# Kernel tuning notes

Measured on AMD Instinct MI355X. Metric: run time of the kernel, lower is better.

The kernel has to match this reference:

```python
import jax, jax.numpy as jnp
import numpy as np

E = 128       # embed_size
H = 256       # hidden_size
Q = 256       # query_size
B = 256       # batch size
N_ENT = 200000
N_REL = 500
N_NODES = 100000   # existing (head) nodes
N_NEW = 50000      # new tail nodes (segment_sum size)
M = 200000         # edges


def setup_inputs() -> dict:
    key = jax.random.key(0)
    ks = jax.random.split(key, 32)
    s = 0.02
    inp = {
        'entity_emb':   jax.random.normal(ks[0], (N_ENT, E), jnp.float32),
        'relation_emb': jax.random.normal(ks[1], (N_REL, E), jnp.float32),
        'node_hidden':  jax.random.normal(ks[2], (N_NODES, H), jnp.float32),
        'query_repr':   jax.random.normal(ks[3], (B, Q), jnp.float32),
        # attention params (Ws_attn, Wr_attn, Wqr_attn, w_alpha)
        'Ws':  jax.random.normal(ks[4], (H, H), jnp.float32) * s,
        'Wr':  jax.random.normal(ks[5], (E, H), jnp.float32) * s,
        'Wqr': jax.random.normal(ks[6], (E, H), jnp.float32) * s,
        'bqr': jnp.zeros((H,), jnp.float32),
        'w_alpha': jax.random.normal(ks[7], (H, 1), jnp.float32) * s,
        'b_alpha': jnp.zeros((1,), jnp.float32),
        # GRUCell (input = 2E message, hidden = H), torch layout [3H, in]
        'W_ih': jax.random.normal(ks[8], (3 * H, 2 * E), jnp.float32) * s,
        'W_hh': jax.random.normal(ks[9], (3 * H, H), jnp.float32) * s,
        'b_ih': jnp.zeros((3 * H,), jnp.float32),
        'b_hh': jnp.zeros((3 * H,), jnp.float32),
        # We2h: entity embed -> initial hidden
        'We2h_W': jax.random.normal(ks[10], (E, H), jnp.float32) * s,
        'We2h_b': jnp.zeros((H,), jnp.float32),
        # candidate_layer: [2E + H] -> H (agent_num = 1)
        'cand_W': jax.random.normal(ks[11], (2 * E + H, H), jnp.float32) * s,
        'cand_b': jnp.zeros((H,), jnp.float32),
        # rank_layer: [H + Q] -> 1
        'rank_W': jax.random.normal(ks[12], (H + Q, 1), jnp.float32) * s,
        'rank_b': jnp.zeros((1,), jnp.float32),
        # LayerNorm
        'ln_g': jnp.ones((H,), jnp.float32),
        'ln_b': jnp.zeros((H,), jnp.float32),
        # edge list (int constants)
        'head_node':     jax.random.randint(ks[13], (M,), 0, N_NODES, jnp.int32),
        'edge_rel':      jax.random.randint(ks[14], (M,), 0, N_REL, jnp.int32),
        'tail_ent':      jax.random.randint(ks[15], (M,), 0, N_ENT, jnp.int32),
        'tail_node':     jax.random.randint(ks[16], (M,), 0, N_NEW, jnp.int32),
        'query_rel':     jax.random.randint(ks[17], (M,), 0, N_REL, jnp.int32),
        'batch_idx':     jax.random.randint(ks[18], (M,), 0, B, jnp.int32),
        'tail_node_ent': jax.random.randint(ks[19], (N_NEW,), 0, N_ENT, jnp.int32),
    }
    return inp


def reference(entity_emb, relation_emb, node_hidden, query_repr,
              Ws, Wr, Wqr, bqr, w_alpha, b_alpha,
              W_ih, W_hh, b_ih, b_hh, We2h_W, We2h_b,
              cand_W, cand_b, rank_W, rank_b, ln_g, ln_b,
              head_node, edge_rel, tail_ent, tail_node, query_rel,
              batch_idx, tail_node_ent):
    lrelu = lambda x: jax.nn.leaky_relu(x, 0.01)
    # --- per-edge attention: w_alpha(ReLU(Ws h_s + Wr h_r + Wqr h_q)) ---
    hs = node_hidden[head_node]            # [M, H]
    hr = relation_emb[edge_rel]            # [M, E]
    hq = relation_emb[query_rel]           # [M, E]
    attn_feat = jax.nn.relu(hs @ Ws + hr @ Wr + hq @ Wqr + bqr)   # [M, H]
    alpha = jax.nn.sigmoid(attn_feat @ w_alpha + b_alpha)         # [M, 1]
    # --- attention-weighted message (rel || tail entity) scattered to tails ---
    te = entity_emb[tail_ent]                                     # [M, E]
    msg = jnp.concatenate([hr, te], axis=-1) * alpha              # [M, 2E]
    agg = jax.ops.segment_sum(msg, tail_node, num_segments=N_NEW) # [N_NEW, 2E]
    # --- GRUCell update of tail-node hidden states ---
    h_prev = lrelu(entity_emb[tail_node_ent] @ We2h_W + We2h_b)   # [N_NEW, H]
    gx = agg @ W_ih.T + b_ih                                      # [N_NEW, 3H]
    gh = h_prev @ W_hh.T + b_hh
    xr, xz, xn = jnp.split(gx, 3, axis=-1)
    hr_, hz_, hn_ = jnp.split(gh, 3, axis=-1)
    r = jax.nn.sigmoid(xr + hr_)
    z = jax.nn.sigmoid(xz + hz_)
    n = jnp.tanh(xn + r * hn_)
    h_new = (1.0 - z) * n + z * h_prev                            # [N_NEW, H]
    mu = jnp.mean(h_new, axis=-1, keepdims=True)
    var = jnp.var(h_new, axis=-1, keepdims=True)
    h_new = (h_new - mu) * jax.lax.rsqrt(var + 1e-5) * ln_g + ln_b
    # --- candidate scoring: candidate_layer + rank_layer ---
    cand_in = jnp.concatenate([te, hr, h_new[tail_node]], axis=-1)   # [M, 2E+H]
    cand_h = lrelu(cand_in @ cand_W + cand_b)                        # [M, H]
    rank_in = jnp.concatenate([cand_h, query_repr[batch_idx]], -1)   # [M, H+Q]
    scores = (rank_in @ rank_W + rank_b)[:, 0]                       # [M]
    return scores
```

## Files before the change

### kernel.cpp

```cpp
#include <hip/hip_runtime.h>
#include <math.h>


#define ACT_NONE 0
#define ACT_LRELU 1

typedef __attribute__((ext_vector_type(8))) short short8;
typedef __attribute__((ext_vector_type(4))) float floatx4;

__device__ __forceinline__ ushort f2b(float x) {
    union { float f; unsigned u; } v; v.f = x;
    return (ushort)((v.u + 0x7fffu + ((v.u >> 16) & 1u)) >> 16);
}
__device__ __forceinline__ float b2f(ushort b) {
    union { unsigned u; float f; } v; v.u = ((unsigned)b) << 16;
    return v.f;
}
__device__ __forceinline__ void gload16(const ushort* g, ushort* l) {
    __builtin_amdgcn_global_load_lds(
        (const __attribute__((address_space(1))) void*)g,
        (__attribute__((address_space(3))) void*)l, 16, 0, 0);
}

__global__ __launch_bounds__(256) void gemm_k(
    const float* __restrict__ A, const float* __restrict__ B,
    const float* __restrict__ bias, float* __restrict__ C,
    int M, int N, int K, const int* __restrict__ a_idx, int act)
{
    __shared__ float As[16][68];
    __shared__ float Bs[16][68];
    const int tid = threadIdx.x;
    const int tx = tid & 15, ty = tid >> 4;
    const int m0 = blockIdx.x * 64, n0 = blockIdx.y * 64;
    float acc[4][4] = {};
    const int ar  = tid >> 2;
    const int ac4 = (tid & 3) * 4;
    const int brow = tid >> 4;
    const int bc4  = (tid & 15) * 4;
    const int gm = m0 + ar;
    const float* Arow = nullptr;
    if (gm < M) {
        int r = a_idx ? a_idx[gm] : gm;
        Arow = A + (size_t)r * K;
    }
    for (int k0 = 0; k0 < K; k0 += 16) {
        float4 av = make_float4(0.f, 0.f, 0.f, 0.f);
        if (Arow) av = *(const float4*)(Arow + k0 + ac4);
        As[ac4 + 0][ar] = av.x;
        As[ac4 + 1][ar] = av.y;
        As[ac4 + 2][ar] = av.z;
        As[ac4 + 3][ar] = av.w;
        float4 bv = *(const float4*)(B + (size_t)(k0 + brow) * N + n0 + bc4);
        *(float4*)&Bs[brow][bc4] = bv;
        __syncthreads();
        #pragma unroll
        for (int kk = 0; kk < 16; ++kk) {
            float4 a4 = *(float4*)&As[kk][ty << 2];
            float4 b4 = *(float4*)&Bs[kk][tx << 2];
            float avr[4] = {a4.x, a4.y, a4.z, a4.w};
            float bvr[4] = {b4.x, b4.y, b4.z, b4.w};
            #pragma unroll
            for (int i = 0; i < 4; ++i)
                #pragma unroll
                for (int j = 0; j < 4; ++j)
                    acc[i][j] = fmaf(avr[i], bvr[j], acc[i][j]);
        }
        __syncthreads();
    }
    const int n = n0 + (tx << 2);
    float4 bv4 = make_float4(0.f, 0.f, 0.f, 0.f);
    if (bias) bv4 = *(const float4*)(bias + n);
    #pragma unroll
    for (int i = 0; i < 4; ++i) {
        int m = m0 + (ty << 2) + i;
        if (m >= M) continue;
        float v0 = acc[i][0] + bv4.x;
        float v1 = acc[i][1] + bv4.y;
        float v2 = acc[i][2] + bv4.z;
        float v3 = acc[i][3] + bv4.w;
        if (act == ACT_LRELU) {
            v0 = v0 > 0.f ? v0 : 0.01f * v0;
            v1 = v1 > 0.f ? v1 : 0.01f * v1;
            v2 = v2 > 0.f ? v2 : 0.01f * v2;
            v3 = v3 > 0.f ? v3 : 0.01f * v3;
        }
        *(float4*)(C + (size_t)m * N + n) = make_float4(v0, v1, v2, v3);
    }
}

__global__ __launch_bounds__(256) void convert16_k(
    const float* __restrict__ in, ushort* __restrict__ out, int n)
{
    int i = blockIdx.x * 256 + threadIdx.x;
    if (i < n) out[i] = f2b(in[i]);
}

__global__ __launch_bounds__(256) void transpose16_k(
    const float* __restrict__ in, ushort* __restrict__ out, int k0, int KS, int N)
{
    int i = blockIdx.x * 256 + threadIdx.x;
    if (i >= KS * N) return;
    int k = i / N, n = i - k * N;
    out[(size_t)n * KS + k] = f2b(in[(size_t)(k0 + k) * N + n]);
}

__global__ __launch_bounds__(256) void gemm16_k(
    const float* __restrict__ A, const int* __restrict__ a_idx,
    const ushort* __restrict__ A16,
    const ushort* __restrict__ BT, const float* __restrict__ bias,
    float* __restrict__ C, ushort* __restrict__ C16,
    int M, int N, int K, int act)
{
    __shared__ ushort As[128 * 40];
    __shared__ ushort Bs[128 * 40];
    const int tid = threadIdx.x;
    const int m0 = blockIdx.x * 128, n0 = blockIdx.y * 128;

    const int rowbase = tid >> 3, f4 = tid & 7;
    const float* arow[4] = {nullptr, nullptr, nullptr, nullptr};
    const int rb16 = tid >> 2, seg16 = tid & 3;
    const ushort* a16row[2] = {nullptr, nullptr};
    if (A16) {
        #pragma unroll
        for (int i = 0; i < 2; ++i) {
            int r = m0 + rb16 + i * 64;
            if (r < M) {
                int rr = a_idx ? a_idx[r] : r;
                a16row[i] = A16 + (size_t)rr * K;
            }
        }
    } else {
        #pragma unroll
        for (int i = 0; i < 4; ++i) {
            int r = m0 + rowbase + i * 32;
            if (r < M) {
                int rr = a_idx ? a_idx[r] : r;
                arow[i] = A + (size_t)rr * K;
            }
        }
    }
    const int brow = tid >> 2, bseg = tid & 3;

    const int l = tid & 63, w = tid >> 6;
    const int wm = (w & 1) * 64, wn = (w >> 1) * 64;
    const int cl = l & 15, q = l >> 4;
    const int aoff = (wm + cl) * 40 + q * 8;
    const int boff = (wn + cl) * 40 + q * 8;

    floatx4 acc[4][4];
    #pragma unroll
    for (int mi = 0; mi < 4; ++mi)
        #pragma unroll
        for (int ni = 0; ni < 4; ++ni) acc[mi][ni] = 0.f;

    for (int k0 = 0; k0 < K; k0 += 32) {
        if (A16) {
            #pragma unroll
            for (int i = 0; i < 2; ++i) {
                uint4 raw = make_uint4(0u, 0u, 0u, 0u);
                if (a16row[i]) raw = *(const uint4*)(a16row[i] + k0 + seg16 * 8);
                *(uint4*)&As[(rb16 + i * 64) * 40 + seg16 * 8] = raw;
            }
        } else {
            #pragma unroll
            for (int i = 0; i < 4; ++i) {
                float4 v = make_float4(0.f, 0.f, 0.f, 0.f);
                if (arow[i]) v = *(const float4*)(arow[i] + k0 + f4 * 4);
                ushort4 b4;
                b4.x = f2b(v.x); b4.y = f2b(v.y); b4.z = f2b(v.z); b4.w = f2b(v.w);
                *(ushort4*)&As[(rowbase + i * 32) * 40 + f4 * 4] = b4;
            }
        }
        #pragma unroll
        for (int i = 0; i < 2; ++i) {
            int r = brow + i * 64;
            uint4 raw = *(const uint4*)(BT + (size_t)(n0 + r) * K + k0 + bseg * 8);
            *(uint4*)&Bs[r * 40 + bseg * 8] = raw;
        }
        __syncthreads();
        short8 af[4], bf[4];
        #pragma unroll
        for (int mi = 0; mi < 4; ++mi) af[mi] = *(short8*)&As[aoff + mi * 640];
        #pragma unroll
        for (int ni = 0; ni < 4; ++ni) bf[ni] = *(short8*)&Bs[boff + ni * 640];
        #pragma unroll
        for (int mi = 0; mi < 4; ++mi)
            #pragma unroll
            for (int ni = 0; ni < 4; ++ni)
                acc[mi][ni] = __builtin_amdgcn_mfma_f32_16x16x32_bf16(
                    bf[ni], af[mi], acc[mi][ni], 0, 0, 0);
        __syncthreads();
    }

    #pragma unroll
    for (int mi = 0; mi < 4; ++mi) {
        int row = m0 + wm + mi * 16 + cl;
        if (row >= M) continue;
        #pragma unroll
        for (int ni = 0; ni < 4; ++ni) {
            int col = n0 + wn + ni * 16 + q * 4;
            float4 bv = bias ? *(const float4*)(bias + col)
                             : make_float4(0.f, 0.f, 0.f, 0.f);
            float v[4];
            #pragma unroll
            for (int r = 0; r < 4; ++r) {
                float x = acc[mi][ni][r] + ((const float*)&bv)[r];
                if (act == ACT_LRELU) x = x > 0.f ? x : 0.01f * x;
                v[r] = x;
            }
            if (C16) {
                ushort4 u;
                u.x = f2b(v[0]); u.y = f2b(v[1]); u.z = f2b(v[2]); u.w = f2b(v[3]);
                *(ushort4*)(C16 + (size_t)row * N + col) = u;
            }
            if (C) *(float4*)(C + (size_t)row * N + col) =
                       make_float4(v[0], v[1], v[2], v[3]);
        }
    }
}

__global__ __launch_bounds__(256) void gemm16p_k(
    const ushort* __restrict__ A16, const int* __restrict__ a_idx,
    const ushort* __restrict__ BT, const float* __restrict__ bias,
    float* __restrict__ C, ushort* __restrict__ C16,
    int M, int N, int K, int act)
{
    __shared__ ushort As[2][128 * 32];
    __shared__ ushort Bs[2][128 * 32];
    const int tid = threadIdx.x;
    const int l = tid & 63, w = tid >> 6;
    const int m0 = blockIdx.y * 128, n0 = blockIdx.x * 128;

    const ushort* agp[2];
    const ushort* bgp[2];
    #pragma unroll
    for (int j = 0; j < 2; ++j) {
        int row = j * 64 + w * 16 + (l >> 2);
        int seg = (l & 3) ^ (row & 3);
        int r = m0 + row; if (r >= M) r = M - 1;
        int rr = a_idx ? a_idx[r] : r;
        agp[j] = A16 + (size_t)rr * K + seg * 8;
        bgp[j] = BT + (size_t)(n0 + row) * K + seg * 8;
    }

    const int wm = (w & 1) * 64, wn = (w >> 1) * 64;
    const int cl = l & 15, q = l >> 4;
    const int sseg = (q ^ (cl & 3)) * 8;
    const int aoff = (wm + cl) * 32 + sseg;
    const int boff = (wn + cl) * 32 + sseg;

    floatx4 acc[4][4];
    #pragma unroll
    for (int mi = 0; mi < 4; ++mi)
        #pragma unroll
        for (int ni = 0; ni < 4; ++ni) acc[mi][ni] = 0.f;

    const int NT = K >> 5;
    #pragma unroll
    for (int j = 0; j < 2; ++j) {
        gload16(agp[j], &As[0][j * 2048 + w * 512]);
        gload16(bgp[j], &Bs[0][j * 2048 + w * 512]);
    }
    __syncthreads();

    int buf = 0;
    for (int t = 0; t < NT; ++t) {
        if (t + 1 < NT) {
            int k0 = (t + 1) * 32;
            #pragma unroll
            for (int j = 0; j < 2; ++j) {
                gload16(agp[j] + k0, &As[buf ^ 1][j * 2048 + w * 512]);
                gload16(bgp[j] + k0, &Bs[buf ^ 1][j * 2048 + w * 512]);
            }
        }
        short8 af[4], bf[4];
        #pragma unroll
        for (int mi = 0; mi < 4; ++mi) af[mi] = *(short8*)&As[buf][aoff + mi * 512];
        #pragma unroll
        for (int ni = 0; ni < 4; ++ni) bf[ni] = *(short8*)&Bs[buf][boff + ni * 512];
        #pragma unroll
        for (int mi = 0; mi < 4; ++mi)
            #pragma unroll
            for (int ni = 0; ni < 4; ++ni)
                acc[mi][ni] = __builtin_amdgcn_mfma_f32_16x16x32_bf16(
                    bf[ni], af[mi], acc[mi][ni], 0, 0, 0);
        __syncthreads();
        buf ^= 1;
    }

    #pragma unroll
    for (int mi = 0; mi < 4; ++mi) {
        int row = m0 + wm + mi * 16 + cl;
        if (row >= M) continue;
        #pragma unroll
        for (int ni = 0; ni < 4; ++ni) {
            int col = n0 + wn + ni * 16 + q * 4;
            float4 bv = bias ? *(const float4*)(bias + col)
                             : make_float4(0.f, 0.f, 0.f, 0.f);
            float v[4];
            #pragma unroll
            for (int r = 0; r < 4; ++r) {
                float x = acc[mi][ni][r] + ((const float*)&bv)[r];
                if (act == ACT_LRELU) x = x > 0.f ? x : 0.01f * x;
                v[r] = x;
            }
            if (C16) {
                ushort4 u;
                u.x = f2b(v[0]); u.y = f2b(v[1]); u.z = f2b(v[2]); u.w = f2b(v[3]);
                *(ushort4*)(C16 + (size_t)row * N + col) = u;
            }
            if (C) *(float4*)(C + (size_t)row * N + col) =
                       make_float4(v[0], v[1], v[2], v[3]);
        }
    }
}

__global__ __launch_bounds__(256) void qdot_k(
    const float* __restrict__ q, const float* __restrict__ rank_W,
    float* __restrict__ qdot)
{
    int b = blockIdx.x * 4 + (threadIdx.x >> 6);
    int l = threadIdx.x & 63;
    float s = 0.f;
    #pragma unroll
    for (int k = 0; k < 4; ++k) {
        int h = l + k * 64;
        s += q[(size_t)b * 256 + h] * rank_W[256 + h];
    }
    #pragma unroll
    for (int off = 32; off; off >>= 1) s += __shfl_xor(s, off, 64);
    if (l == 0) qdot[b] = s;
}

__global__ __launch_bounds__(256) void alpha_k(
    const ushort* __restrict__ nodeWs16, const float* __restrict__ relWr,
    const float* __restrict__ relWqr, const float* __restrict__ bqr,
    const float* __restrict__ w_alpha, const float* __restrict__ b_alpha_p,
    const int* __restrict__ head_node, const int* __restrict__ edge_rel,
    const int* __restrict__ query_rel, float* __restrict__ alpha_out)
{
    const int tid = threadIdx.x;
    const int e0 = blockIdx.x * 32;
    __shared__ int hn[32], er[32], qr[32];
    if (tid < 32) {
        int e = e0 + tid;
        hn[tid] = head_node[e]; er[tid] = edge_rel[e]; qr[tid] = query_rel[e];
    }
    __syncthreads();
    const int tx = tid & 63, ty = tid >> 6;
    const int c = tx * 4;
    const float4 bq = *(const float4*)(bqr + c);
    const float4 wa = *(const float4*)(w_alpha + c);
    float part[8];
    #pragma unroll
    for (int i2 = 0; i2 < 8; ++i2) {
        int i = ty * 8 + i2;
        ushort4 a16 = *(const ushort4*)(nodeWs16 + (size_t)hn[i] * 256 + c);
        float4 b = *(const float4*)(relWr + (size_t)er[i] * 256 + c);
        float4 d = *(const float4*)(relWqr + (size_t)qr[i] * 256 + c);
        float x0 = fmaxf(b2f(a16.x) + b.x + d.x + bq.x, 0.f);
        float x1 = fmaxf(b2f(a16.y) + b.y + d.y + bq.y, 0.f);
        float x2 = fmaxf(b2f(a16.z) + b.z + d.z + bq.z, 0.f);
        float x3 = fmaxf(b2f(a16.w) + b.w + d.w + bq.w, 0.f);
        part[i2] = x0 * wa.x + x1 * wa.y + x2 * wa.z + x3 * wa.w;
    }
    #pragma unroll
    for (int off = 32; off; off >>= 1)
        #pragma unroll
        for (int i2 = 0; i2 < 8; ++i2)
            part[i2] += __shfl_xor(part[i2], off, 64);
    if (tx == 0) {
        float ba = b_alpha_p[0];
        #pragma unroll
        for (int i2 = 0; i2 < 8; ++i2)
            alpha_out[e0 + ty * 8 + i2] = 1.f / (1.f + __expf(-(part[i2] + ba)));
    }
}

__global__ __launch_bounds__(256) void hist_k(
    const int* __restrict__ tail_node, int* __restrict__ deg, int M)
{
    int e = blockIdx.x * 256 + threadIdx.x;
    if (e < M) atomicAdd(&deg[tail_node[e]], 1);
}
__global__ __launch_bounds__(256) void scan1_k(
    const int* __restrict__ deg, int* __restrict__ partial, int N)
{
    __shared__ int sm[256];
    int i = blockIdx.x * 256 + threadIdx.x;
    int v = (i < N) ? deg[i] : 0;
    sm[threadIdx.x] = v;
    __syncthreads();
    for (int off = 128; off; off >>= 1) {
        if (threadIdx.x < off) sm[threadIdx.x] += sm[threadIdx.x + off];
        __syncthreads();
    }
    if (threadIdx.x == 0) partial[blockIdx.x] = sm[0];
}
__global__ __launch_bounds__(256) void scan2_k(
    int* __restrict__ partial, int nPart, int* __restrict__ offsets, int N, int M)
{
    __shared__ int sm[256];
    int t = threadIdx.x;
    int v = (t < nPart) ? partial[t] : 0;
    sm[t] = v;
    __syncthreads();
    for (int off = 1; off < 256; off <<= 1) {
        int add = (t >= off) ? sm[t - off] : 0;
        __syncthreads();
        sm[t] += add;
        __syncthreads();
    }
    if (t < nPart) partial[t] = sm[t] - v;
    if (t == 0) offsets[N] = M;
}
__global__ __launch_bounds__(256) void scan3_k(
    const int* __restrict__ deg, const int* __restrict__ partial,
    int* __restrict__ offsets, int* __restrict__ cursor, int N)
{
    __shared__ int sm[256];
    int i = blockIdx.x * 256 + threadIdx.x;
    int t = threadIdx.x;
    int v = (i < N) ? deg[i] : 0;
    sm[t] = v;
    __syncthreads();
    for (int off = 1; off < 256; off <<= 1) {
        int add = (t >= off) ? sm[t - off] : 0;
        __syncthreads();
        sm[t] += add;
        __syncthreads();
    }
    if (i < N) {
        int excl = partial[blockIdx.x] + sm[t] - v;
        offsets[i] = excl;
        cursor[i] = excl;
    }
}
__global__ __launch_bounds__(256) void fill_k(
    const int* __restrict__ tail_node, int* __restrict__ cursor,
    int* __restrict__ csr, int M)
{
    int e = blockIdx.x * 256 + threadIdx.x;
    if (e < M) {
        int pos = atomicAdd(&cursor[tail_node[e]], 1);
        csr[pos] = e;
    }
}

__global__ __launch_bounds__(256) void agg_csr_k(
    const float* __restrict__ relation_emb, const ushort* __restrict__ ent16,
    const float* __restrict__ alpha, const int* __restrict__ edge_rel,
    const int* __restrict__ tail_ent, const int* __restrict__ offsets,
    const int* __restrict__ csr, ushort* __restrict__ agg16)
{
    int node = blockIdx.x * 4 + (threadIdx.x >> 6);
    int lane = threadIdx.x & 63;
    int beg = offsets[node], end = offsets[node + 1];
    float4 acc = make_float4(0.f, 0.f, 0.f, 0.f);
    const int c = lane * 4;
    for (int j = beg; j < end; ++j) {
        int e = csr[j];
        float a = alpha[e];
        float4 v;
        if (lane < 32) {
            v = *(const float4*)(relation_emb + (size_t)edge_rel[e] * 128 + c);
        } else {
            ushort4 u = *(const ushort4*)(ent16 + (size_t)tail_ent[e] * 128 + (c - 128));
            v = make_float4(b2f(u.x), b2f(u.y), b2f(u.z), b2f(u.w));
        }
        acc.x += v.x * a; acc.y += v.y * a;
        acc.z += v.z * a; acc.w += v.w * a;
    }
    ushort4 o;
    o.x = f2b(acc.x); o.y = f2b(acc.y); o.z = f2b(acc.z); o.w = f2b(acc.w);
    *(ushort4*)(agg16 + (size_t)node * 256 + c) = o;
}

__global__ __launch_bounds__(256) void gru_ln_k(
    const float* __restrict__ gx, const float* __restrict__ gh,
    const float* __restrict__ h_prev, const float* __restrict__ ln_g,
    const float* __restrict__ ln_b, ushort* __restrict__ h_new16, int n0)
{
    int nl = blockIdx.x * 4 + (threadIdx.x >> 6);
    int lane = threadIdx.x & 63;
    int n = n0 + nl;
    const float* gxr = gx + (size_t)nl * 768;
    const float* ghr = gh + (size_t)nl * 768;
    const float* hpr = h_prev + (size_t)n * 256;
    float hv[4]; float s = 0.f, s2 = 0.f;
    #pragma unroll
    for (int q2 = 0; q2 < 4; ++q2) {
        int h = lane + q2 * 64;
        float xr = gxr[h], xz = gxr[256 + h], xn = gxr[512 + h];
        float hr_ = ghr[h], hz_ = ghr[256 + h], hn_ = ghr[512 + h];
        float hp = hpr[h];
        float r = 1.f / (1.f + __expf(-(xr + hr_)));
        float z = 1.f / (1.f + __expf(-(xz + hz_)));
        float nn = tanhf(xn + r * hn_);
        float v = (1.f - z) * nn + z * hp;
        hv[q2] = v; s += v; s2 += v * v;
    }
    #pragma unroll
    for (int off = 32; off; off >>= 1) {
        s  += __shfl_xor(s, off, 64);
        s2 += __shfl_xor(s2, off, 64);
    }
    float mean = s * (1.f / 256.f);
    float var  = s2 * (1.f / 256.f) - mean * mean;
    float rstd = rsqrtf(var + 1e-5f);
    ushort* outr = h_new16 + (size_t)n * 256;
    #pragma unroll
    for (int q2 = 0; q2 < 4; ++q2) {
        int h = lane + q2 * 64;
        outr[h] = f2b((hv[q2] - mean) * rstd * ln_g[h] + ln_b[h]);
    }
}

__global__ __launch_bounds__(256) void score_mfma_k(
    const ushort* __restrict__ ent16, const ushort* __restrict__ candW1T,
    const ushort* __restrict__ relCand16, const ushort* __restrict__ hnewCand16,
    const float* __restrict__ rank_W, const float* __restrict__ rank_b_p,
    const float* __restrict__ qdot, const int* __restrict__ csr,
    const int* __restrict__ tail_ent, const int* __restrict__ edge_rel,
    const int* __restrict__ tail_node, const int* __restrict__ batch_idx,
    float* __restrict__ scores)
{
    __shared__ ushort As[64 * 136];
    __shared__ int s_e[64], s_te[64], s_er[64], s_tn[64], s_bi[64];
    __shared__ float s_part[4][64];
    const int tid = threadIdx.x;
    const int e0 = blockIdx.x * 64;
    if (tid < 64) {
        int e = csr[e0 + tid];
        s_e[tid] = e;
        s_te[tid] = tail_ent[e]; s_er[tid] = edge_rel[e];
        s_tn[tid] = tail_node[e]; s_bi[tid] = batch_idx[e];
    }
    __syncthreads();

    {
        const int row = tid >> 2, s0 = tid & 3;
        const ushort* ar = ent16 + (size_t)s_te[row] * 128;
        #pragma unroll
        for (int j = 0; j < 4; ++j) {
            int seg = s0 + j * 4;
            *(uint4*)&As[row * 136 + seg * 8] = *(const uint4*)(ar + seg * 8);
        }
    }
    __syncthreads();

    const int l = tid & 63, w = tid >> 6;
    const int cl = l & 15, q = l >> 4;

    floatx4 acc[4][4];
    #pragma unroll
    for (int mi = 0; mi < 4; ++mi)
        #pragma unroll
        for (int ni = 0; ni < 4; ++ni) acc[mi][ni] = 0.f;

    const ushort* bbase = candW1T + (size_t)(w * 64 + cl) * 128 + q * 8;

    for (int k0 = 0; k0 < 128; k0 += 32) {
        short8 af[4], bf[4];
        #pragma unroll
        for (int ni = 0; ni < 4; ++ni)
            bf[ni] = *(const short8*)(bbase + ni * 2048 + k0);
        #pragma unroll
        for (int mi = 0; mi < 4; ++mi)
            af[mi] = *(short8*)&As[(mi * 16 + cl) * 136 + k0 + q * 8];
        #pragma unroll
        for (int mi = 0; mi < 4; ++mi)
            #pragma unroll
            for (int ni = 0; ni < 4; ++ni)
                acc[mi][ni] = __builtin_amdgcn_mfma_f32_16x16x32_bf16(
                    bf[ni], af[mi], acc[mi][ni], 0, 0, 0);
    }

    float rowsum[4];
    #pragma unroll
    for (int mi = 0; mi < 4; ++mi) {
        int row = mi * 16 + cl;
        int er = s_er[row], tn = s_tn[row];
        float rs = 0.f;
        #pragma unroll
        for (int ni = 0; ni < 4; ++ni) {
            int col = w * 64 + ni * 16 + q * 4;
            ushort4 rc = *(const ushort4*)(relCand16 + (size_t)er * 256 + col);
            ushort4 hc = *(const ushort4*)(hnewCand16 + (size_t)tn * 256 + col);
            float4 rw = *(const float4*)(rank_W + col);
            float v0 = acc[mi][ni][0] + b2f(rc.x) + b2f(hc.x);
            float v1 = acc[mi][ni][1] + b2f(rc.y) + b2f(hc.y);
            float v2 = acc[mi][ni][2] + b2f(rc.z) + b2f(hc.z);
            float v3 = acc[mi][ni][3] + b2f(rc.w) + b2f(hc.w);
            v0 = v0 > 0.f ? v0 : 0.01f * v0;
            v1 = v1 > 0.f ? v1 : 0.01f * v1;
            v2 = v2 > 0.f ? v2 : 0.01f * v2;
            v3 = v3 > 0.f ? v3 : 0.01f * v3;
            rs += v0 * rw.x + v1 * rw.y + v2 * rw.z + v3 * rw.w;
        }
        rowsum[mi] = rs;
    }
    #pragma unroll
    for (int mi = 0; mi < 4; ++mi) {
        rowsum[mi] += __shfl_xor(rowsum[mi], 16, 64);
        rowsum[mi] += __shfl_xor(rowsum[mi], 32, 64);
    }
    if (q == 0) {
        #pragma unroll
        for (int mi = 0; mi < 4; ++mi)
            s_part[w][mi * 16 + cl] = rowsum[mi];
    }
    __syncthreads();
    if (tid < 64) {
        float s = s_part[0][tid] + s_part[1][tid] + s_part[2][tid] + s_part[3][tid]
                + qdot[s_bi[tid]] + rank_b_p[0];
        scores[s_e[tid]] = s;
    }
}

extern "C" void kernel_launch(void* const* d_in, const int* in_sizes, int n_in,
                              void* d_out, int out_size, void* d_ws, size_t ws_size,
                              hipStream_t stream)
{
    const float* entity_emb   = (const float*)d_in[0];
    const float* relation_emb = (const float*)d_in[1];
    const float* node_hidden  = (const float*)d_in[2];
    const float* query_repr   = (const float*)d_in[3];
    const float* Ws    = (const float*)d_in[4];
    const float* Wr    = (const float*)d_in[5];
    const float* Wqr   = (const float*)d_in[6];
    const float* bqr   = (const float*)d_in[7];
    const float* w_alpha = (const float*)d_in[8];
    const float* b_alpha = (const float*)d_in[9];
    const float* W_ih  = (const float*)d_in[10];
    const float* W_hh  = (const float*)d_in[11];
    const float* b_ih  = (const float*)d_in[12];
    const float* b_hh  = (const float*)d_in[13];
    const float* We2h_W = (const float*)d_in[14];
    const float* We2h_b = (const float*)d_in[15];
    const float* cand_W = (const float*)d_in[16];
    const float* cand_b = (const float*)d_in[17];
    const float* rank_W = (const float*)d_in[18];
    const float* rank_b = (const float*)d_in[19];
    const float* ln_g  = (const float*)d_in[20];
    const float* ln_b  = (const float*)d_in[21];
    const int* head_node = (const int*)d_in[22];
    const int* edge_rel  = (const int*)d_in[23];
    const int* tail_ent  = (const int*)d_in[24];
    const int* tail_node = (const int*)d_in[25];
    const int* query_rel = (const int*)d_in[26];
    const int* batch_idx = (const int*)d_in[27];
    const int* tail_node_ent = (const int*)d_in[28];
    float* out = (float*)d_out;
    (void)in_sizes; (void)n_in; (void)out_size; (void)ws_size;

    const int M = 200000, NNEW = 50000, NNODES = 100000, NREL = 500;
    const int NENT = 200000, E = 128;
    const int NCHUNK = 4, NC = NNEW / NCHUNK;
    const int NPART = (NNEW + 255) / 256;

    float* w = (float*)d_ws;
    float* relWr    = w; w += NREL * 256;
    float* relWqr   = w; w += NREL * 256;
    float* relCand  = w; w += NREL * 256;
    float* qdot     = w; w += 256;
    float* alpha    = w; w += M;
    float* h_prev   = w; w += (size_t)NNEW * 256;
    ushort* agg16      = (ushort*)w; w += (size_t)NNEW * 256 / 2;
    ushort* hnewCand16 = (ushort*)w; w += (size_t)NNEW * 256 / 2;
    ushort* relCand16  = (ushort*)w; w += (NREL * 256) / 2;
    ushort* ent16      = (ushort*)w; w += (size_t)NENT * E / 2;
    ushort* h_new16    = (ushort*)w; w += (size_t)NNEW * 256 / 2;
    ushort* W_ih16    = (ushort*)w; w += (768 * 256) / 2;
    ushort* W_hh16    = (ushort*)w; w += (768 * 256) / 2;
    ushort* WsT16     = (ushort*)w; w += (256 * 256) / 2;
    ushort* We2hT16   = (ushort*)w; w += (256 * 128) / 2;
    ushort* candW1T16 = (ushort*)w; w += (256 * 128) / 2;
    ushort* candW3T16 = (ushort*)w; w += (256 * 256) / 2;
    int* deg     = (int*)w; w += NNEW;
    int* offsets = (int*)w; w += NNEW + 1;
    int* cursor  = (int*)w; w += NNEW;
    int* partial = (int*)w; w += 256;
    int* csr     = (int*)w; w += M;
    w = (float*)(((uintptr_t)w + 63) & ~(uintptr_t)63);
    float* big = w;
    ushort* nh16     = (ushort*)big;
    ushort* nodeWs16 = (ushort*)big + (size_t)NNODES * 256;
    float* gx_buf = big;
    float* gh_buf = big + (size_t)NC * 768;

    hipMemsetAsync(deg, 0, NNEW * sizeof(int), stream);
    hist_k<<<(M + 255) / 256, 256, 0, stream>>>(tail_node, deg, M);
    scan1_k<<<NPART, 256, 0, stream>>>(deg, partial, NNEW);
    scan2_k<<<1, 256, 0, stream>>>(partial, NPART, offsets, NNEW, M);
    scan3_k<<<NPART, 256, 0, stream>>>(deg, partial, offsets, cursor, NNEW);
    fill_k<<<(M + 255) / 256, 256, 0, stream>>>(tail_node, cursor, csr, M);

    convert16_k<<<(NENT * E + 255) / 256, 256, 0, stream>>>(entity_emb, ent16, NENT * E);
    convert16_k<<<(NNODES * 256 + 255) / 256, 256, 0, stream>>>(node_hidden, nh16, NNODES * 256);
    convert16_k<<<768, 256, 0, stream>>>(W_ih, W_ih16, 768 * 256);
    convert16_k<<<768, 256, 0, stream>>>(W_hh, W_hh16, 768 * 256);
    transpose16_k<<<256, 256, 0, stream>>>(Ws, WsT16, 0, 256, 256);
    transpose16_k<<<128, 256, 0, stream>>>(We2h_W, We2hT16, 0, 128, 256);
    transpose16_k<<<128, 256, 0, stream>>>(cand_W, candW1T16, 0, 128, 256);
    transpose16_k<<<256, 256, 0, stream>>>(cand_W, candW3T16, 256, 256, 256);
    gemm_k<<<dim3(8, 4), 256, 0, stream>>>(relation_emb, Wr,  nullptr, relWr,  NREL, 256, 128, nullptr, ACT_NONE);
    gemm_k<<<dim3(8, 4), 256, 0, stream>>>(relation_emb, Wqr, nullptr, relWqr, NREL, 256, 128, nullptr, ACT_NONE);
    gemm_k<<<dim3(8, 4), 256, 0, stream>>>(relation_emb, cand_W + 128 * 256, nullptr, relCand, NREL, 256, 128, nullptr, ACT_NONE);
    convert16_k<<<(NREL * 256 + 255) / 256, 256, 0, stream>>>(relCand, relCand16, NREL * 256);
    qdot_k<<<64, 256, 0, stream>>>(query_repr, rank_W, qdot);

    gemm16p_k<<<dim3(2, (NNODES + 127) / 128), 256, 0, stream>>>(
        nh16, nullptr, WsT16, nullptr, nullptr, nodeWs16, NNODES, 256, 256, ACT_NONE);

    alpha_k<<<M / 32, 256, 0, stream>>>(nodeWs16, relWr, relWqr, bqr, w_alpha, b_alpha,
                                        head_node, edge_rel, query_rel, alpha);

    agg_csr_k<<<NNEW / 4, 256, 0, stream>>>(relation_emb, ent16, alpha,
                                            edge_rel, tail_ent, offsets, csr, agg16);

    gemm16p_k<<<dim3(2, (NNEW + 127) / 128), 256, 0, stream>>>(
        ent16, tail_node_ent, We2hT16, We2h_b, h_prev, nullptr, NNEW, 256, 128, ACT_LRELU);

    for (int ch = 0; ch < NCHUNK; ++ch) {
        int n0 = ch * NC;
        gemm16p_k<<<dim3(6, (NC + 127) / 128), 256, 0, stream>>>(
            agg16 + (size_t)n0 * 256, nullptr, W_ih16, b_ih, gx_buf, nullptr, NC, 768, 256, ACT_NONE);
        gemm16_k<<<dim3((NC + 127) / 128, 6), 256, 0, stream>>>(
            h_prev + (size_t)n0 * 256, nullptr, nullptr, W_hh16, b_hh, gh_buf, nullptr, NC, 768, 256, ACT_NONE);
        gru_ln_k<<<NC / 4, 256, 0, stream>>>(gx_buf, gh_buf, h_prev, ln_g, ln_b, h_new16, n0);
    }

    gemm16p_k<<<dim3(2, (NNEW + 127) / 128), 256, 0, stream>>>(
        h_new16, nullptr, candW3T16, cand_b, nullptr, hnewCand16, NNEW, 256, 256, ACT_NONE);

    score_mfma_k<<<M / 64, 256, 0, stream>>>(ent16, candW1T16, relCand16, hnewCand16,
                                             rank_W, rank_b, qdot, csr, tail_ent,
                                             edge_rel, tail_node, batch_idx, out);
}
```

Baseline: 915.8 us.

## Sort edges by head node, store GRU intermediates in bf16, fuse fp32 convert into GEMM

Builds a second CSR keyed on head node so alpha_k gathers nodeWs rows in sorted order, and materializes permuted edge attributes so later kernels read them sequentially. Replaces the separate node_hidden bf16 conversion with a GEMM that converts fp32 A tiles on the fly. Stores h_prev, gx and gh in bf16 and runs the W_hh GEMM through the pipelined kernel. It also widens the scan blocks and reworks score_mfma_k to handle 128 edges per block. The aim is less memory traffic and better gather locality, at the cost of extra sort passes and lower intermediate precision.

```diff
diff --git a/kernel.cpp b/kernel.cpp
--- a/kernel.cpp
+++ b/kernel.cpp
@@ -94,7 +94,6 @@
     int i = blockIdx.x * 256 + threadIdx.x;
     if (i < n) out[i] = f2b(in[i]);
 }
-
 __global__ __launch_bounds__(256) void transpose16_k(
     const float* __restrict__ in, ushort* __restrict__ out, int k0, int KS, int N)
 {
@@ -104,48 +103,35 @@
     out[(size_t)n * KS + k] = f2b(in[(size_t)(k0 + k) * N + n]);
 }
 
-__global__ __launch_bounds__(256) void gemm16_k(
-    const float* __restrict__ A, const int* __restrict__ a_idx,
-    const ushort* __restrict__ A16,
+__global__ __launch_bounds__(256) void gemm16p_k(
+    const ushort* __restrict__ A16, const int* __restrict__ a_idx,
     const ushort* __restrict__ BT, const float* __restrict__ bias,
     float* __restrict__ C, ushort* __restrict__ C16,
     int M, int N, int K, int act)
 {
-    __shared__ ushort As[128 * 40];
-    __shared__ ushort Bs[128 * 40];
+    __shared__ ushort As[2][128 * 32];
+    __shared__ ushort Bs[2][128 * 32];
     const int tid = threadIdx.x;
-    const int m0 = blockIdx.x * 128, n0 = blockIdx.y * 128;
-
-    const int rowbase = tid >> 3, f4 = tid & 7;
-    const float* arow[4] = {nullptr, nullptr, nullptr, nullptr};
-    const int rb16 = tid >> 2, seg16 = tid & 3;
-    const ushort* a16row[2] = {nullptr, nullptr};
-    if (A16) {
-        #pragma unroll
-        for (int i = 0; i < 2; ++i) {
-            int r = m0 + rb16 + i * 64;
-            if (r < M) {
-                int rr = a_idx ? a_idx[r] : r;
-                a16row[i] = A16 + (size_t)rr * K;
-            }
-        }
-    } else {
-        #pragma unroll
-        for (int i = 0; i < 4; ++i) {
-            int r = m0 + rowbase + i * 32;
-            if (r < M) {
-                int rr = a_idx ? a_idx[r] : r;
-                arow[i] = A + (size_t)rr * K;
-            }
-        }
-    }
-    const int brow = tid >> 2, bseg = tid & 3;
-
     const int l = tid & 63, w = tid >> 6;
+    const int m0 = blockIdx.y * 128, n0 = blockIdx.x * 128;
+
+    const ushort* agp[2];
+    const ushort* bgp[2];
+    #pragma unroll
+    for (int j = 0; j < 2; ++j) {
+        int row = j * 64 + w * 16 + (l >> 2);
+        int seg = (l & 3) ^ (row & 3);
+        int r = m0 + row; if (r >= M) r = M - 1;
+        int rr = a_idx ? a_idx[r] : r;
+        agp[j] = A16 + (size_t)rr * K + seg * 8;
+        bgp[j] = BT + (size_t)(n0 + row) * K + seg * 8;
+    }
+
     const int wm = (w & 1) * 64, wn = (w >> 1) * 64;
     const int cl = l & 15, q = l >> 4;
-    const int aoff = (wm + cl) * 40 + q * 8;
-    const int boff = (wn + cl) * 40 + q * 8;
+    const int sseg = (q ^ (cl & 3)) * 8;
+    const int aoff = (wm + cl) * 32 + sseg;
+    const int boff = (wn + cl) * 32 + sseg;
 
     floatx4 acc[4][4];
     #pragma unroll
@@ -153,36 +139,29 @@
         #pragma unroll
         for (int ni = 0; ni < 4; ++ni) acc[mi][ni] = 0.f;
 
-    for (int k0 = 0; k0 < K; k0 += 32) {
-        if (A16) {
-            #pragma unroll
-            for (int i = 0; i < 2; ++i) {
-                uint4 raw = make_uint4(0u, 0u, 0u, 0u);
-                if (a16row[i]) raw = *(const uint4*)(a16row[i] + k0 + seg16 * 8);
-                *(uint4*)&As[(rb16 + i * 64) * 40 + seg16 * 8] = raw;
+    const int NT = K >> 5;
+    #pragma unroll
+    for (int j = 0; j < 2; ++j) {
+        gload16(agp[j], &As[0][j * 2048 + w * 512]);
+        gload16(bgp[j], &Bs[0][j * 2048 + w * 512]);
+    }
+    __syncthreads();
+
+    int buf = 0;
+    for (int t = 0; t < NT; ++t) {
+        if (t + 1 < NT) {
+            int k0 = (t + 1) * 32;
+            #pragma unroll
+            for (int j = 0; j < 2; ++j) {
+                gload16(agp[j] + k0, &As[buf ^ 1][j * 2048 + w * 512]);
+                gload16(bgp[j] + k0, &Bs[buf ^ 1][j * 2048 + w * 512]);
             }
-        } else {
-            #pragma unroll
-            for (int i = 0; i < 4; ++i) {
-                float4 v = make_float4(0.f, 0.f, 0.f, 0.f);
-                if (arow[i]) v = *(const float4*)(arow[i] + k0 + f4 * 4);
-                ushort4 b4;
-                b4.x = f2b(v.x); b4.y = f2b(v.y); b4.z = f2b(v.z); b4.w = f2b(v.w);
-                *(ushort4*)&As[(rowbase + i * 32) * 40 + f4 * 4] = b4;
-            }
-        }
-        #pragma unroll
-        for (int i = 0; i < 2; ++i) {
-            int r = brow + i * 64;
-            uint4 raw = *(const uint4*)(BT + (size_t)(n0 + r) * K + k0 + bseg * 8);
-            *(uint4*)&Bs[r * 40 + bseg * 8] = raw;
-        }
-        __syncthreads();
+        }
         short8 af[4], bf[4];
         #pragma unroll
-        for (int mi = 0; mi < 4; ++mi) af[mi] = *(short8*)&As[aoff + mi * 640];
-        #pragma unroll
-        for (int ni = 0; ni < 4; ++ni) bf[ni] = *(short8*)&Bs[boff + ni * 640];
+        for (int mi = 0; mi < 4; ++mi) af[mi] = *(short8*)&As[buf][aoff + mi * 512];
+        #pragma unroll
+        for (int ni = 0; ni < 4; ++ni) bf[ni] = *(short8*)&Bs[buf][boff + ni * 512];
         #pragma unroll
         for (int mi = 0; mi < 4; ++mi)
             #pragma unroll
@@ -190,6 +169,7 @@
                 acc[mi][ni] = __builtin_amdgcn_mfma_f32_16x16x32_bf16(
                     bf[ni], af[mi], acc[mi][ni], 0, 0, 0);
         __syncthreads();
+        buf ^= 1;
     }
 
     #pragma unroll
@@ -219,10 +199,9 @@
     }
 }
 
-__global__ __launch_bounds__(256) void gemm16p_k(
-    const ushort* __restrict__ A16, const int* __restrict__ a_idx,
-    const ushort* __restrict__ BT, const float* __restrict__ bias,
-    float* __restrict__ C, ushort* __restrict__ C16,
+__global__ __launch_bounds__(256) void gemm16pf_k(
+    const float* __restrict__ A, const ushort* __restrict__ BT,
+    const float* __restrict__ bias, ushort* __restrict__ C16,
     int M, int N, int K, int act)
 {
     __shared__ ushort As[2][128 * 32];
@@ -231,15 +210,21 @@
     const int l = tid & 63, w = tid >> 6;
     const int m0 = blockIdx.y * 128, n0 = blockIdx.x * 128;
 
-    const ushort* agp[2];
+    const int rowbase = tid >> 3, f4 = tid & 7;
+    const float* arow[4];
+    int awadr[4];
+    #pragma unroll
+    for (int i = 0; i < 4; ++i) {
+        int row = rowbase + i * 32;
+        int r = m0 + row; if (r >= M) r = M - 1;
+        arow[i] = A + (size_t)r * K;
+        awadr[i] = row * 32 + (((f4 >> 1) ^ (row & 3)) * 8) + (f4 & 1) * 4;
+    }
     const ushort* bgp[2];
     #pragma unroll
     for (int j = 0; j < 2; ++j) {
         int row = j * 64 + w * 16 + (l >> 2);
         int seg = (l & 3) ^ (row & 3);
-        int r = m0 + row; if (r >= M) r = M - 1;
-        int rr = a_idx ? a_idx[r] : r;
-        agp[j] = A16 + (size_t)rr * K + seg * 8;
         bgp[j] = BT + (size_t)(n0 + row) * K + seg * 8;
     }
 
@@ -257,21 +242,26 @@
 
     const int NT = K >> 5;
     #pragma unroll
-    for (int j = 0; j < 2; ++j) {
-        gload16(agp[j], &As[0][j * 2048 + w * 512]);
-        gload16(bgp[j], &Bs[0][j * 2048 + w * 512]);
+    for (int j = 0; j < 2; ++j) gload16(bgp[j], &Bs[0][j * 2048 + w * 512]);
+    #pragma unroll
+    for (int i = 0; i < 4; ++i) {
+        float4 v = *(const float4*)(arow[i] + f4 * 4);
+        ushort4 u; u.x = f2b(v.x); u.y = f2b(v.y); u.z = f2b(v.z); u.w = f2b(v.w);
+        *(ushort4*)&As[0][awadr[i]] = u;
     }
     __syncthreads();
 
     int buf = 0;
     for (int t = 0; t < NT; ++t) {
+        float4 av[4];
         if (t + 1 < NT) {
             int k0 = (t + 1) * 32;
             #pragma unroll
-            for (int j = 0; j < 2; ++j) {
-                gload16(agp[j] + k0, &As[buf ^ 1][j * 2048 + w * 512]);
+            for (int j = 0; j < 2; ++j)
                 gload16(bgp[j] + k0, &Bs[buf ^ 1][j * 2048 + w * 512]);
-            }
+            #pragma unroll
+            for (int i = 0; i < 4; ++i)
+                av[i] = *(const float4*)(arow[i] + k0 + f4 * 4);
         }
         short8 af[4], bf[4];
         #pragma unroll
@@ -284,6 +274,15 @@
             for (int ni = 0; ni < 4; ++ni)
                 acc[mi][ni] = __builtin_amdgcn_mfma_f32_16x16x32_bf16(
                     bf[ni], af[mi], acc[mi][ni], 0, 0, 0);
+        if (t + 1 < NT) {
+            #pragma unroll
+            for (int i = 0; i < 4; ++i) {
+                ushort4 u;
+                u.x = f2b(av[i].x); u.y = f2b(av[i].y);
+                u.z = f2b(av[i].z); u.w = f2b(av[i].w);
+                *(ushort4*)&As[buf ^ 1][awadr[i]] = u;
+            }
+        }
         __syncthreads();
         buf ^= 1;
     }
@@ -297,20 +296,19 @@
             int col = n0 + wn + ni * 16 + q * 4;
             float4 bv = bias ? *(const float4*)(bias + col)
                              : make_float4(0.f, 0.f, 0.f, 0.f);
-            float v[4];
-            #pragma unroll
-            for (int r = 0; r < 4; ++r) {
-                float x = acc[mi][ni][r] + ((const float*)&bv)[r];
-                if (act == ACT_LRELU) x = x > 0.f ? x : 0.01f * x;
-                v[r] = x;
+            ushort4 u;
+            float x0 = acc[mi][ni][0] + bv.x;
+            float x1 = acc[mi][ni][1] + bv.y;
+            float x2 = acc[mi][ni][2] + bv.z;
+            float x3 = acc[mi][ni][3] + bv.w;
+            if (act == ACT_LRELU) {
+                x0 = x0 > 0.f ? x0 : 0.01f * x0;
+                x1 = x1 > 0.f ? x1 : 0.01f * x1;
+                x2 = x2 > 0.f ? x2 : 0.01f * x2;
+                x3 = x3 > 0.f ? x3 : 0.01f * x3;
             }
-            if (C16) {
-                ushort4 u;
-                u.x = f2b(v[0]); u.y = f2b(v[1]); u.z = f2b(v[2]); u.w = f2b(v[3]);
-                *(ushort4*)(C16 + (size_t)row * N + col) = u;
-            }
-            if (C) *(float4*)(C + (size_t)row * N + col) =
-                       make_float4(v[0], v[1], v[2], v[3]);
+            u.x = f2b(x0); u.y = f2b(x1); u.z = f2b(x2); u.w = f2b(x3);
+            *(ushort4*)(C16 + (size_t)row * N + col) = u;
         }
     }
 }
@@ -336,15 +334,17 @@
     const ushort* __restrict__ nodeWs16, const float* __restrict__ relWr,
     const float* __restrict__ relWqr, const float* __restrict__ bqr,
     const float* __restrict__ w_alpha, const float* __restrict__ b_alpha_p,
-    const int* __restrict__ head_node, const int* __restrict__ edge_rel,
-    const int* __restrict__ query_rel, float* __restrict__ alpha_out)
+    const int* __restrict__ hcsr_hn, const int* __restrict__ hcsr_er,
+    const int* __restrict__ hcsr_qr, const int* __restrict__ hcsr_e,
+    float* __restrict__ alpha_out)
 {
     const int tid = threadIdx.x;
     const int e0 = blockIdx.x * 32;
-    __shared__ int hn[32], er[32], qr[32];
+    __shared__ int hn[32], er[32], qr[32], se[32];
     if (tid < 32) {
-        int e = e0 + tid;
-        hn[tid] = head_node[e]; er[tid] = edge_rel[e]; qr[tid] = query_rel[e];
+        int i = e0 + tid;
+        hn[tid] = hcsr_hn[i]; er[tid] = hcsr_er[i];
+        qr[tid] = hcsr_qr[i]; se[tid] = hcsr_e[i];
     }
     __syncthreads();
     const int tx = tid & 63, ty = tid >> 6;
@@ -373,25 +373,24 @@
         float ba = b_alpha_p[0];
         #pragma unroll
         for (int i2 = 0; i2 < 8; ++i2)
-            alpha_out[e0 + ty * 8 + i2] = 1.f / (1.f + __expf(-(part[i2] + ba)));
+            alpha_out[se[ty * 8 + i2]] = 1.f / (1.f + __expf(-(part[i2] + ba)));
     }
 }
 
 __global__ __launch_bounds__(256) void hist_k(
-    const int* __restrict__ tail_node, int* __restrict__ deg, int M)
+    const int* __restrict__ key, int* __restrict__ deg, int M)
 {
     int e = blockIdx.x * 256 + threadIdx.x;
-    if (e < M) atomicAdd(&deg[tail_node[e]], 1);
-}
-__global__ __launch_bounds__(256) void scan1_k(
+    if (e < M) atomicAdd(&deg[key[e]], 1);
+}
+__global__ __launch_bounds__(512) void scan1_k(
     const int* __restrict__ deg, int* __restrict__ partial, int N)
 {
-    __shared__ int sm[256];
-    int i = blockIdx.x * 256 + threadIdx.x;
-    int v = (i < N) ? deg[i] : 0;
-    sm[threadIdx.x] = v;
+    __shared__ int sm[512];
+    int i = blockIdx.x * 512 + threadIdx.x;
+    sm[threadIdx.x] = (i < N) ? deg[i] : 0;
     __syncthreads();
-    for (int off = 128; off; off >>= 1) {
+    for (int off = 256; off; off >>= 1) {
         if (threadIdx.x < off) sm[threadIdx.x] += sm[threadIdx.x + off];
         __syncthreads();
     }
@@ -414,17 +413,17 @@
     if (t < nPart) partial[t] = sm[t] - v;
     if (t == 0) offsets[N] = M;
 }
-__global__ __launch_bounds__(256) void scan3_k(
+__global__ __launch_bounds__(512) void scan3_k(
     const int* __restrict__ deg, const int* __restrict__ partial,
     int* __restrict__ offsets, int* __restrict__ cursor, int N)
 {
-    __shared__ int sm[256];
-    int i = blockIdx.x * 256 + threadIdx.x;
+    __shared__ int sm[512];
+    int i = blockIdx.x * 512 + threadIdx.x;
     int t = threadIdx.x;
     int v = (i < N) ? deg[i] : 0;
     sm[t] = v;
     __syncthreads();
-    for (int off = 1; off < 256; off <<= 1) {
+    for (int off = 1; off < 512; off <<= 1) {
         int add = (t >= off) ? sm[t - off] : 0;
         __syncthreads();
         sm[t] += add;
@@ -437,21 +436,38 @@
     }
 }
 __global__ __launch_bounds__(256) void fill_k(
-    const int* __restrict__ tail_node, int* __restrict__ cursor,
-    int* __restrict__ csr, int M)
+    const int* __restrict__ tail_node, const int* __restrict__ tail_ent,
+    const int* __restrict__ edge_rel, const int* __restrict__ batch_idx,
+    int* __restrict__ cursor, int* __restrict__ ce, int* __restrict__ cte,
+    int* __restrict__ cer, int* __restrict__ ctn, int* __restrict__ cbi, int M)
 {
     int e = blockIdx.x * 256 + threadIdx.x;
     if (e < M) {
-        int pos = atomicAdd(&cursor[tail_node[e]], 1);
-        csr[pos] = e;
+        int tn = tail_node[e];
+        int pos = atomicAdd(&cursor[tn], 1);
+        ce[pos] = e; cte[pos] = tail_ent[e]; cer[pos] = edge_rel[e];
+        ctn[pos] = tn; cbi[pos] = batch_idx[e];
+    }
+}
+__global__ __launch_bounds__(256) void hfill_k(
+    const int* __restrict__ head_node, const int* __restrict__ edge_rel,
+    const int* __restrict__ query_rel, int* __restrict__ cursor,
+    int* __restrict__ hhn, int* __restrict__ her, int* __restrict__ hqr,
+    int* __restrict__ he, int M)
+{
+    int e = blockIdx.x * 256 + threadIdx.x;
+    if (e < M) {
+        int h = head_node[e];
+        int pos = atomicAdd(&cursor[h], 1);
+        hhn[pos] = h; her[pos] = edge_rel[e]; hqr[pos] = query_rel[e]; he[pos] = e;
     }
 }
 
 __global__ __launch_bounds__(256) void agg_csr_k(
     const float* __restrict__ relation_emb, const ushort* __restrict__ ent16,
-    const float* __restrict__ alpha, const int* __restrict__ edge_rel,
-    const int* __restrict__ tail_ent, const int* __restrict__ offsets,
-    const int* __restrict__ csr, ushort* __restrict__ agg16)
+    const float* __restrict__ alpha, const int* __restrict__ csr_e,
+    const int* __restrict__ csr_er, const int* __restrict__ csr_te,
+    const int* __restrict__ offsets, ushort* __restrict__ agg16)
 {
     int node = blockIdx.x * 4 + (threadIdx.x >> 6);
     int lane = threadIdx.x & 63;
@@ -459,13 +475,12 @@
     float4 acc = make_float4(0.f, 0.f, 0.f, 0.f);
     const int c = lane * 4;
     for (int j = beg; j < end; ++j) {
-        int e = csr[j];
-        float a = alpha[e];
+        float a = alpha[csr_e[j]];
         float4 v;
         if (lane < 32) {
-            v = *(const float4*)(relation_emb + (size_t)edge_rel[e] * 128 + c);
+            v = *(const float4*)(relation_emb + (size_t)csr_er[j] * 128 + c);
         } else {
-            ushort4 u = *(const ushort4*)(ent16 + (size_t)tail_ent[e] * 128 + (c - 128));
+            ushort4 u = *(const ushort4*)(ent16 + (size_t)csr_te[j] * 128 + (c - 128));
             v = make_float4(b2f(u.x), b2f(u.y), b2f(u.z), b2f(u.w));
         }
         acc.x += v.x * a; acc.y += v.y * a;
@@ -477,23 +492,24 @@
 }
 
 __global__ __launch_bounds__(256) void gru_ln_k(
-    const float* __restrict__ gx, const float* __restrict__ gh,
-    const float* __restrict__ h_prev, const float* __restrict__ ln_g,
+    const ushort* __restrict__ gx, const ushort* __restrict__ gh,
+    const ushort* __restrict__ h_prev, const float* __restrict__ ln_g,
     const float* __restrict__ ln_b, ushort* __restrict__ h_new16, int n0)
 {
     int nl = blockIdx.x * 4 + (threadIdx.x >> 6);
     int lane = threadIdx.x & 63;
     int n = n0 + nl;
-    const float* gxr = gx + (size_t)nl * 768;
-    const float* ghr = gh + (size_t)nl * 768;
-    const float* hpr = h_prev + (size_t)n * 256;
+    const ushort* gxr = gx + (size_t)nl * 768;
+    const ushort* ghr = gh + (size_t)nl * 768;
+    const ushort* hpr = h_prev + (size_t)n * 256;
     float hv[4]; float s = 0.f, s2 = 0.f;
     #pragma unroll
     for (int q2 = 0; q2 < 4; ++q2) {
         int h = lane + q2 * 64;
-        float xr = gxr[h], xz = gxr[256 + h], xn = gxr[512 + h];
-        float hr_ = ghr[h], hz_ = ghr[256 + h], hn_ = ghr[512 + h];
-        float hp = hpr[h];
+        float xr = b2f(gxr[h]), xz = b2f(gxr[256 + h]), xn = b2f(gxr[512 + h]);
+        float hr_ = b2f(ghr[h]), hn_ = b2f(ghr[512 + h]);
+        float hz_ = b2f(ghr[256 + h]);
+        float hp = b2f(hpr[h]);
         float r = 1.f / (1.f + __expf(-(xr + hr_)));
         float z = 1.f / (1.f + __expf(-(xz + hz_)));
         float nn = tanhf(xn + r * hn_);
@@ -520,31 +536,33 @@
     const ushort* __restrict__ ent16, const ushort* __restrict__ candW1T,
     const ushort* __restrict__ relCand16, const ushort* __restrict__ hnewCand16,
     const float* __restrict__ rank_W, const float* __restrict__ rank_b_p,
-    const float* __restrict__ qdot, const int* __restrict__ csr,
-    const int* __restrict__ tail_ent, const int* __restrict__ edge_rel,
-    const int* __restrict__ tail_node, const int* __restrict__ batch_idx,
-    float* __restrict__ scores)
-{
-    __shared__ ushort As[64 * 136];
-    __shared__ int s_e[64], s_te[64], s_er[64], s_tn[64], s_bi[64];
-    __shared__ float s_part[4][64];
+    const float* __restrict__ qdot,
+    const int* __restrict__ csr_e, const int* __restrict__ csr_te,
+    const int* __restrict__ csr_er, const int* __restrict__ csr_tn,
+    const int* __restrict__ csr_bi, float* __restrict__ scores, int M)
+{
+    __shared__ ushort As[128 * 136];
+    __shared__ int s_er[128], s_tn[128];
+    __shared__ float s_part[4][128];
     const int tid = threadIdx.x;
-    const int e0 = blockIdx.x * 64;
-    if (tid < 64) {
-        int e = csr[e0 + tid];
-        s_e[tid] = e;
-        s_te[tid] = tail_ent[e]; s_er[tid] = edge_rel[e];
-        s_tn[tid] = tail_node[e]; s_bi[tid] = batch_idx[e];
-    }
-    __syncthreads();
-
+    const int e0 = blockIdx.x * 128;
+    int cnt = M - e0; if (cnt > 128) cnt = 128;
+
+    if (tid < 128) {
+        int idx = e0 + (tid < cnt ? tid : 0);
+        s_er[tid] = csr_er[idx];
+        s_tn[tid] = csr_tn[idx];
+    }
     {
-        const int row = tid >> 2, s0 = tid & 3;
-        const ushort* ar = ent16 + (size_t)s_te[row] * 128;
-        #pragma unroll
-        for (int j = 0; j < 4; ++j) {
-            int seg = s0 + j * 4;
-            *(uint4*)&As[row * 136 + seg * 8] = *(const uint4*)(ar + seg * 8);
+        int row = tid >> 1;
+        int idx = e0 + (row < cnt ? row : 0);
+        const ushort* ar = ent16 + (size_t)csr_te[idx] * 128;
+        int s0 = (tid & 1) * 8;
+        #pragma unroll
+        for (int j = 0; j < 8; ++j) {
+            int seg = s0 + j;
+            int slot = seg ^ (row & 3);
+            *(uint4*)&As[row * 136 + slot * 8] = *(const uint4*)(ar + seg * 8);
         }
     }
     __syncthreads();
@@ -552,69 +570,74 @@
     const int l = tid & 63, w = tid >> 6;
     const int cl = l & 15, q = l >> 4;
 
-    floatx4 acc[4][4];
-    #pragma unroll
-    for (int mi = 0; mi < 4; ++mi)
-        #pragma unroll
-        for (int ni = 0; ni < 4; ++ni) acc[mi][ni] = 0.f;
-
-    const ushort* bbase = candW1T + (size_t)(w * 64 + cl) * 128 + q * 8;
-
-    for (int k0 = 0; k0 < 128; k0 += 32) {
-        short8 af[4], bf[4];
-        #pragma unroll
-        for (int ni = 0; ni < 4; ++ni)
-            bf[ni] = *(const short8*)(bbase + ni * 2048 + k0);
-        #pragma unroll
-        for (int mi = 0; mi < 4; ++mi)
-            af[mi] = *(short8*)&As[(mi * 16 + cl) * 136 + k0 + q * 8];
-        #pragma unroll
-        for (int mi = 0; mi < 4; ++mi)
-            #pragma unroll
-            for (int ni = 0; ni < 4; ++ni)
-                acc[mi][ni] = __builtin_amdgcn_mfma_f32_16x16x32_bf16(
-                    bf[ni], af[mi], acc[mi][ni], 0, 0, 0);
-    }
-
-    float rowsum[4];
-    #pragma unroll
-    for (int mi = 0; mi < 4; ++mi) {
-        int row = mi * 16 + cl;
-        int er = s_er[row], tn = s_tn[row];
-        float rs = 0.f;
-        #pragma unroll
-        for (int ni = 0; ni < 4; ++ni) {
-            int col = w * 64 + ni * 16 + q * 4;
-            ushort4 rc = *(const ushort4*)(relCand16 + (size_t)er * 256 + col);
-            ushort4 hc = *(const ushort4*)(hnewCand16 + (size_t)tn * 256 + col);
-            float4 rw = *(const float4*)(rank_W + col);
-            float v0 = acc[mi][ni][0] + b2f(rc.x) + b2f(hc.x);
-            float v1 = acc[mi][ni][1] + b2f(rc.y) + b2f(hc.y);
-            float v2 = acc[mi][ni][2] + b2f(rc.z) + b2f(hc.z);
-            float v3 = acc[mi][ni][3] + b2f(rc.w) + b2f(hc.w);
-            v0 = v0 > 0.f ? v0 : 0.01f * v0;
-            v1 = v1 > 0.f ? v1 : 0.01f * v1;
-            v2 = v2 > 0.f ? v2 : 0.01f * v2;
-            v3 = v3 > 0.f ? v3 : 0.01f * v3;
-            rs += v0 * rw.x + v1 * rw.y + v2 * rw.z + v3 * rw.w;
-        }
-        rowsum[mi] = rs;
-    }
-    #pragma unroll
-    for (int mi = 0; mi < 4; ++mi) {
+    float rowsum[8];
+    #pragma unroll
+    for (int mi = 0; mi < 8; ++mi) rowsum[mi] = 0.f;
+
+    #pragma unroll
+    for (int ch = 0; ch < 2; ++ch) {
+        floatx4 acc[8][2];
+        #pragma unroll
+        for (int mi = 0; mi < 8; ++mi)
+            #pragma unroll
+            for (int ni = 0; ni < 2; ++ni) acc[mi][ni] = 0.f;
+
+        const ushort* bb = candW1T + (size_t)(w * 64 + ch * 32 + cl) * 128 + q * 8;
+        #pragma unroll
+        for (int k0 = 0; k0 < 128; k0 += 32) {
+            short8 bf[2];
+            #pragma unroll
+            for (int ni = 0; ni < 2; ++ni)
+                bf[ni] = *(const short8*)(bb + ni * 2048 + k0);
+            #pragma unroll
+            for (int mi = 0; mi < 8; ++mi) {
+                int row = mi * 16 + cl;
+                int slot = (((k0 >> 3) + q) ^ (cl & 3));
+                short8 af = *(short8*)&As[row * 136 + slot * 8];
+                #pragma unroll
+                for (int ni = 0; ni < 2; ++ni)
+                    acc[mi][ni] = __builtin_amdgcn_mfma_f32_16x16x32_bf16(
+                        bf[ni], af, acc[mi][ni], 0, 0, 0);
+            }
+        }
+        #pragma unroll
+        for (int mi = 0; mi < 8; ++mi) {
+            int row = mi * 16 + cl;
+            int er = s_er[row], tn = s_tn[row];
+            #pragma unroll
+            for (int ni = 0; ni < 2; ++ni) {
+                int col = w * 64 + ch * 32 + ni * 16 + q * 4;
+                ushort4 rc = *(const ushort4*)(relCand16 + (size_t)er * 256 + col);
+                ushort4 hc = *(const ushort4*)(hnewCand16 + (size_t)tn * 256 + col);
+                float4 rw = *(const float4*)(rank_W + col);
+                float v0 = acc[mi][ni][0] + b2f(rc.x) + b2f(hc.x);
+                float v1 = acc[mi][ni][1] + b2f(rc.y) + b2f(hc.y);
+                float v2 = acc[mi][ni][2] + b2f(rc.z) + b2f(hc.z);
+                float v3 = acc[mi][ni][3] + b2f(rc.w) + b2f(hc.w);
+                v0 = v0 > 0.f ? v0 : 0.01f * v0;
+                v1 = v1 > 0.f ? v1 : 0.01f * v1;
+                v2 = v2 > 0.f ? v2 : 0.01f * v2;
+                v3 = v3 > 0.f ? v3 : 0.01f * v3;
+                rowsum[mi] += v0 * rw.x + v1 * rw.y + v2 * rw.z + v3 * rw.w;
+            }
+        }
+    }
+    #pragma unroll
+    for (int mi = 0; mi < 8; ++mi) {
         rowsum[mi] += __shfl_xor(rowsum[mi], 16, 64);
         rowsum[mi] += __shfl_xor(rowsum[mi], 32, 64);
     }
     if (q == 0) {
         #pragma unroll
-        for (int mi = 0; mi < 4; ++mi)
+        for (int mi = 0; mi < 8; ++mi)
             s_part[w][mi * 16 + cl] = rowsum[mi];
     }
     __syncthreads();
-    if (tid < 64) {
+    if (tid < cnt) {
+        int idx = e0 + tid;
         float s = s_part[0][tid] + s_part[1][tid] + s_part[2][tid] + s_part[3][tid]
-                + qdot[s_bi[tid]] + rank_b_p[0];
-        scores[s_e[tid]] = s;
+                + qdot[csr_bi[idx]] + rank_b_p[0];
+        scores[csr_e[idx]] = s;
     }
 }
 
@@ -657,7 +680,8 @@
     const int M = 200000, NNEW = 50000, NNODES = 100000, NREL = 500;
     const int NENT = 200000, E = 128;
     const int NCHUNK = 4, NC = NNEW / NCHUNK;
-    const int NPART = (NNEW + 255) / 256;
+    const int NP_T = (NNEW + 511) / 512;
+    const int NP_H = (NNODES + 511) / 512;
 
     float* w = (float*)d_ws;
     float* relWr    = w; w += NREL * 256;
@@ -665,7 +689,7 @@
     float* relCand  = w; w += NREL * 256;
     float* qdot     = w; w += 256;
     float* alpha    = w; w += M;
-    float* h_prev   = w; w += (size_t)NNEW * 256;
+    ushort* h_prev16   = (ushort*)w; w += (size_t)NNEW * 256 / 2;
     ushort* agg16      = (ushort*)w; w += (size_t)NNEW * 256 / 2;
     ushort* hnewCand16 = (ushort*)w; w += (size_t)NNEW * 256 / 2;
     ushort* relCand16  = (ushort*)w; w += (NREL * 256) / 2;
@@ -677,27 +701,44 @@
     ushort* We2hT16   = (ushort*)w; w += (256 * 128) / 2;
     ushort* candW1T16 = (ushort*)w; w += (256 * 128) / 2;
     ushort* candW3T16 = (ushort*)w; w += (256 * 256) / 2;
-    int* deg     = (int*)w; w += NNEW;
-    int* offsets = (int*)w; w += NNEW + 1;
-    int* cursor  = (int*)w; w += NNEW;
-    int* partial = (int*)w; w += 256;
-    int* csr     = (int*)w; w += M;
+    int* deg      = (int*)w; w += NNEW;
+    int* offsets  = (int*)w; w += NNEW + 1;
+    int* cursor   = (int*)w; w += NNEW;
+    int* deg2     = (int*)w; w += NNODES;
+    int* offsets2 = (int*)w; w += NNODES + 1;
+    int* cursor2  = (int*)w; w += NNODES;
+    int* partial  = (int*)w; w += 512;
+    int* csr_e  = (int*)w; w += M;
+    int* csr_te = (int*)w; w += M;
+    int* csr_er = (int*)w; w += M;
+    int* csr_tn = (int*)w; w += M;
+    int* csr_bi = (int*)w; w += M;
+    int* hcsr_hn = (int*)w; w += M;
+    int* hcsr_er = (int*)w; w += M;
+    int* hcsr_qr = (int*)w; w += M;
+    int* hcsr_e  = (int*)w; w += M;
     w = (float*)(((uintptr_t)w + 63) & ~(uintptr_t)63);
     float* big = w;
-    ushort* nh16     = (ushort*)big;
-    ushort* nodeWs16 = (ushort*)big + (size_t)NNODES * 256;
-    float* gx_buf = big;
-    float* gh_buf = big + (size_t)NC * 768;
+    ushort* nodeWs16 = (ushort*)big;
+    ushort* gx16 = (ushort*)big;
+    ushort* gh16 = (ushort*)big + (size_t)NC * 768;
 
     hipMemsetAsync(deg, 0, NNEW * sizeof(int), stream);
+    hipMemsetAsync(deg2, 0, NNODES * sizeof(int), stream);
     hist_k<<<(M + 255) / 256, 256, 0, stream>>>(tail_node, deg, M);
-    scan1_k<<<NPART, 256, 0, stream>>>(deg, partial, NNEW);
-    scan2_k<<<1, 256, 0, stream>>>(partial, NPART, offsets, NNEW, M);
-    scan3_k<<<NPART, 256, 0, stream>>>(deg, partial, offsets, cursor, NNEW);
-    fill_k<<<(M + 255) / 256, 256, 0, stream>>>(tail_node, cursor, csr, M);
+    scan1_k<<<NP_T, 512, 0, stream>>>(deg, partial, NNEW);
+    scan2_k<<<1, 256, 0, stream>>>(partial, NP_T, offsets, NNEW, M);
+    scan3_k<<<NP_T, 512, 0, stream>>>(deg, partial, offsets, cursor, NNEW);
+    fill_k<<<(M + 255) / 256, 256, 0, stream>>>(tail_node, tail_ent, edge_rel,
+        batch_idx, cursor, csr_e, csr_te, csr_er, csr_tn, csr_bi, M);
+    hist_k<<<(M + 255) / 256, 256, 0, stream>>>(head_node, deg2, M);
+    scan1_k<<<NP_H, 512, 0, stream>>>(deg2, partial, NNODES);
+    scan2_k<<<1, 256, 0, stream>>>(partial, NP_H, offsets2, NNODES, M);
+    scan3_k<<<NP_H, 512, 0, stream>>>(deg2, partial, offsets2, cursor2, NNODES);
+    hfill_k<<<(M + 255) / 256, 256, 0, stream>>>(head_node, edge_rel, query_rel,
+        cursor2, hcsr_hn, hcsr_er, hcsr_qr, hcsr_e, M);
 
     convert16_k<<<(NENT * E + 255) / 256, 256, 0, stream>>>(entity_emb, ent16, NENT * E);
-    convert16_k<<<(NNODES * 256 + 255) / 256, 256, 0, stream>>>(node_hidden, nh16, NNODES * 256);
     convert16_k<<<768, 256, 0, stream>>>(W_ih, W_ih16, 768 * 256);
     convert16_k<<<768, 256, 0, stream>>>(W_hh, W_hh16, 768 * 256);
     transpose16_k<<<256, 256, 0, stream>>>(Ws, WsT16, 0, 256, 256);
@@ -710,31 +751,31 @@
     convert16_k<<<(NREL * 256 + 255) / 256, 256, 0, stream>>>(relCand, relCand16, NREL * 256);
     qdot_k<<<64, 256, 0, stream>>>(query_repr, rank_W, qdot);
 
-    gemm16p_k<<<dim3(2, (NNODES + 127) / 128), 256, 0, stream>>>(
-        nh16, nullptr, WsT16, nullptr, nullptr, nodeWs16, NNODES, 256, 256, ACT_NONE);
+    gemm16pf_k<<<dim3(2, (NNODES + 127) / 128), 256, 0, stream>>>(
+        node_hidden, WsT16, nullptr, nodeWs16, NNODES, 256, 256, ACT_NONE);
 
     alpha_k<<<M / 32, 256, 0, stream>>>(nodeWs16, relWr, relWqr, bqr, w_alpha, b_alpha,
-                                        head_node, edge_rel, query_rel, alpha);
+                                        hcsr_hn, hcsr_er, hcsr_qr, hcsr_e, alpha);
 
     agg_csr_k<<<NNEW / 4, 256, 0, stream>>>(relation_emb, ent16, alpha,
-                                            edge_rel, tail_ent, offsets, csr, agg16);
+                                            csr_e, csr_er, csr_te, offsets, agg16);
 
     gemm16p_k<<<dim3(2, (NNEW + 127) / 128), 256, 0, stream>>>(
-        ent16, tail_node_ent, We2hT16, We2h_b, h_prev, nullptr, NNEW, 256, 128, ACT_LRELU);
+        ent16, tail_node_ent, We2hT16, We2h_b, nullptr, h_prev16, NNEW, 256, 128, ACT_LRELU);
 
     for (int ch = 0; ch < NCHUNK; ++ch) {
         int n0 = ch * NC;
         gemm16p_k<<<dim3(6, (NC + 127) / 128), 256, 0, stream>>>(
-            agg16 + (size_t)n0 * 256, nullptr, W_ih16, b_ih, gx_buf, nullptr, NC, 768, 256, ACT_NONE);
-        gemm16_k<<<dim3((NC + 127) / 128, 6), 256, 0, stream>>>(
-            h_prev + (size_t)n0 * 256, nullptr, nullptr, W_hh16, b_hh, gh_buf, nullptr, NC, 768, 256, ACT_NONE);
-        gru_ln_k<<<NC / 4, 256, 0, stream>>>(gx_buf, gh_buf, h_prev, ln_g, ln_b, h_new16, n0);
+            agg16 + (size_t)n0 * 256, nullptr, W_ih16, b_ih, nullptr, gx16, NC, 768, 256, ACT_NONE);
+        gemm16p_k<<<dim3(6, (NC + 127) / 128), 256, 0, stream>>>(
+            h_prev16 + (size_t)n0 * 256, nullptr, W_hh16, b_hh, nullptr, gh16, NC, 768, 256, ACT_NONE);
+        gru_ln_k<<<NC / 4, 256, 0, stream>>>(gx16, gh16, h_prev16, ln_g, ln_b, h_new16, n0);
     }
 
     gemm16p_k<<<dim3(2, (NNEW + 127) / 128), 256, 0, stream>>>(
         h_new16, nullptr, candW3T16, cand_b, nullptr, hnewCand16, NNEW, 256, 256, ACT_NONE);
 
-    score_mfma_k<<<M / 64, 256, 0, stream>>>(ent16, candW1T16, relCand16, hnewCand16,
-                                             rank_W, rank_b, qdot, csr, tail_ent,
-                                             edge_rel, tail_node, batch_idx, out);
-}
+    score_mfma_k<<<(M + 127) / 128, 256, 0, stream>>>(
+        ent16, candW1T16, relCand16, hnewCand16, rank_W, rank_b, qdot,
+        csr_e, csr_te, csr_er, csr_tn, csr_bi, out, M);
+}
```

Measured after the change: 883.6 us. 3.5% less time.
